# Optimization experiments

Hardware: AMD Instinct MI355X
Metric: run time of the kernel (lower is better)

## Reference

```python
import jax, jax.numpy as jnp
import numpy as np

N_VARS = 512      # code length n (input_output_layer_size)
DV = 4            # variable-node degree
E = N_VARS * DV   # neurons = number of Tanner-graph edges = 2048
B = 8192          # batch of codewords
CLIP_TANH = 10.0
KL_SCALE = 5.0


def _build_masks():
    # edge e belongs to variable node var_idx[e]
    var_idx = np.repeat(np.arange(N_VARS), DV)          # [E]
    same_var = var_idx[:, None] == var_idx[None, :]     # [E,E]
    # v2c (odd->even) mask: edges sharing a variable node, excluding self-edge
    odd2even_mask = (same_var & ~np.eye(E, dtype=bool)).astype(np.float32)
    # skip-connection mask: LLR of variable v feeds every edge incident to v
    skip_mask = (np.arange(N_VARS)[:, None] == var_idx[None, :]).astype(np.float32)  # [n,E]
    return jnp.asarray(odd2even_mask), jnp.asarray(skip_mask)


def setup_inputs() -> dict:
    key = jax.random.key(0)
    k = jax.random.split(key, 6)
    w_odd2even_mask, w_skipconn2even_mask = _build_masks()
    return {
        "x": jax.random.normal(k[0], (B, E), dtype=jnp.float32),
        "llr": jax.random.normal(k[1], (B, N_VARS), dtype=jnp.float32),
        "odd_weights": jax.random.normal(k[2], (E, E), dtype=jnp.float32),
        "llr_weights": jax.random.normal(k[3], (N_VARS, E), dtype=jnp.float32),
        "dropout_logit": jax.random.uniform(k[4], (E,), dtype=jnp.float32),  # torch.rand init
        "u": jax.random.uniform(k[5], (E, E), dtype=jnp.float32),            # ARM uniform noise
        "w_odd2even_mask": w_odd2even_mask,
        "w_skipconn2even_mask": w_skipconn2even_mask,
    }


def reference(x, llr, odd_weights, llr_weights, dropout_logit, u,
              w_odd2even_mask, w_skipconn2even_mask):
    p = jax.nn.sigmoid(dropout_logit)                       # [E], broadcasts over rows of u
    total_mask = w_odd2even_mask * odd_weights              # [E,E]
    # ARM dropout: z ~ (u < sigmoid(logit)), z_tilde ~ (u > sigmoid(-logit))
    z = (u < p).astype(x.dtype)
    z_tilde = (u > jax.nn.sigmoid(-dropout_logit)).astype(x.dtype)
    msgs = x @ (total_mask * z)                             # [B,E]
    msgs_tilde = x @ (total_mask * z_tilde)                 # [B,E]
    llr_term = llr @ (w_skipconn2even_mask * llr_weights)   # [B,E]
    output = jnp.tanh(0.5 * jnp.clip(msgs + llr_term, -CLIP_TANH, CLIP_TANH))
    init_arm_tilde = jnp.tanh(0.5 * jnp.clip(msgs_tilde + llr_term, -CLIP_TANH, CLIP_TANH))
    # KL / entropy regularizer
    scaling1 = (KL_SCALE ** 2 / 2.0) * p                    # [E]
    first_layer_kl = scaling1 * jnp.sum(odd_weights ** 2, axis=1)  # ||W||_2 per row, squared
    H1 = -p * jnp.log(p) - (1.0 - p) * jnp.log(1.0 - p)
    kl_term = jnp.mean(first_layer_kl - H1)
    return output, init_arm_tilde, kl_term
```

## Files before the change

### kernel.cpp

```cpp
#include <hip/hip_runtime.h>
#include <math.h>

#define N_VARS 512
#define DV 4
#define EDGES 2048
#define BATCH 8192
#define CLIP_TANH 10.0f
#define ROWS 8

__global__ __launch_bounds__(256) void precompute_params(
    const float* __restrict__ odd_weights,
    const float* __restrict__ llr_weights,
    const float* __restrict__ dropout_logit,
    const float* __restrict__ u,
    const float* __restrict__ mask_oe,
    const float* __restrict__ mask_skip,
    float4* __restrict__ WZ,
    float4* __restrict__ WZT,
    float*  __restrict__ LW)
{
    int e = blockIdx.x * 256 + threadIdx.x;
    if (e >= EDGES) return;
    int v = e >> 2;
    int base = v << 2;

    float logit = dropout_logit[e];
    float p = 1.0f / (1.0f + expf(-logit));
    float q = 1.0f / (1.0f + expf(logit));

    float wz[4], wzt[4];
#pragma unroll
    for (int j = 0; j < 4; ++j) {
        size_t off = (size_t)(base + j) * EDGES + e;
        float w = odd_weights[off] * mask_oe[off];
        float uu = u[off];
        wz[j]  = (uu < p) ? w : 0.0f;
        wzt[j] = (uu > q) ? w : 0.0f;
    }
    WZ[e]  = make_float4(wz[0], wz[1], wz[2], wz[3]);
    WZT[e] = make_float4(wzt[0], wzt[1], wzt[2], wzt[3]);

    size_t soff = (size_t)v * EDGES + e;
    LW[e] = llr_weights[soff] * mask_skip[soff];
}

__global__ __launch_bounds__(256) void kl_rows(
    const float* __restrict__ odd_weights,
    const float* __restrict__ dropout_logit,
    float* __restrict__ rowv)
{
    int e = blockIdx.x;
    int t = threadIdx.x;
    const float4* row = (const float4*)(odd_weights + (size_t)e * EDGES);
    float s = 0.0f;
#pragma unroll
    for (int i = t; i < EDGES / 4; i += 256) {
        float4 w = row[i];
        s = fmaf(w.x, w.x, s);
        s = fmaf(w.y, w.y, s);
        s = fmaf(w.z, w.z, s);
        s = fmaf(w.w, w.w, s);
    }
#pragma unroll
    for (int off = 32; off > 0; off >>= 1)
        s += __shfl_down(s, off, 64);
    __shared__ float red[4];
    if ((t & 63) == 0) red[t >> 6] = s;
    __syncthreads();
    if (t == 0) {
        float ss = red[0] + red[1] + red[2] + red[3];
        float logit = dropout_logit[e];
        float p = 1.0f / (1.0f + expf(-logit));
        float H1 = -p * logf(p) - (1.0f - p) * logf(1.0f - p);
        rowv[e] = 12.5f * p * ss - H1;
    }
}

__global__ __launch_bounds__(256) void kl_final(
    const float* __restrict__ rowv, float* __restrict__ out)
{
    int t = threadIdx.x;
    float s = 0.0f;
#pragma unroll
    for (int i = t; i < EDGES; i += 256) s += rowv[i];
#pragma unroll
    for (int off = 32; off > 0; off >>= 1)
        s += __shfl_down(s, off, 64);
    __shared__ float red[4];
    if ((t & 63) == 0) red[t >> 6] = s;
    __syncthreads();
    if (t == 0) out[0] = (red[0] + red[1] + red[2] + red[3]) / (float)EDGES;
}

__device__ __forceinline__ float tanh_half(float m) {
    float t = __expf(m);
    return (t - 1.0f) / (t + 1.0f);
}

__global__ __launch_bounds__(256) void main_kernel(
    const float* __restrict__ x,
    const float* __restrict__ llr,
    const float4* __restrict__ WZ,
    const float4* __restrict__ WZT,
    const float*  __restrict__ LW,
    float* __restrict__ out0,
    float* __restrict__ out1)
{
    int idx = blockIdx.x * 256 + threadIdx.x;
    int v = idx & (N_VARS - 1);
    int b0 = (idx >> 9) * ROWS;

    float4 wz[4], wzt[4];
    float lw[4];
#pragma unroll
    for (int c = 0; c < 4; ++c) {
        int e = (v << 2) + c;
        wz[c]  = WZ[e];
        wzt[c] = WZT[e];
        lw[c]  = LW[e];
    }

    float4 x4[ROWS];
    float  l[ROWS];
#pragma unroll
    for (int r = 0; r < ROWS; ++r) {
        x4[r] = ((const float4*)(x + (size_t)(b0 + r) * EDGES))[v];
        l[r]  = llr[(size_t)(b0 + r) * N_VARS + v];
    }

#pragma unroll
    for (int r = 0; r < ROWS; ++r) {
        float o0[4], o1[4];
#pragma unroll
        for (int c = 0; c < 4; ++c) {
            float lt = l[r] * lw[c];
            float m  = fmaf(x4[r].x, wz[c].x,  fmaf(x4[r].y, wz[c].y,
                       fmaf(x4[r].z, wz[c].z,  fmaf(x4[r].w, wz[c].w,  lt))));
            float mt = fmaf(x4[r].x, wzt[c].x, fmaf(x4[r].y, wzt[c].y,
                       fmaf(x4[r].z, wzt[c].z, fmaf(x4[r].w, wzt[c].w, lt))));
            m  = fminf(fmaxf(m,  -CLIP_TANH), CLIP_TANH);
            mt = fminf(fmaxf(mt, -CLIP_TANH), CLIP_TANH);
            o0[c] = tanh_half(m);
            o1[c] = tanh_half(mt);
        }
        ((float4*)(out0 + (size_t)(b0 + r) * EDGES))[v] =
            make_float4(o0[0], o0[1], o0[2], o0[3]);
        ((float4*)(out1 + (size_t)(b0 + r) * EDGES))[v] =
            make_float4(o1[0], o1[1], o1[2], o1[3]);
    }
}

extern "C" void kernel_launch(void* const* d_in, const int* in_sizes, int n_in,
                              void* d_out, int out_size, void* d_ws, size_t ws_size,
                              hipStream_t stream) {
    const float* x             = (const float*)d_in[0];
    const float* llr           = (const float*)d_in[1];
    const float* odd_weights   = (const float*)d_in[2];
    const float* llr_weights   = (const float*)d_in[3];
    const float* dropout_logit = (const float*)d_in[4];
    const float* u             = (const float*)d_in[5];
    const float* mask_oe       = (const float*)d_in[6];
    const float* mask_skip     = (const float*)d_in[7];

    float* out0 = (float*)d_out;
    float* out1 = out0 + (size_t)BATCH * EDGES;
    float* kl   = out0 + (size_t)2 * BATCH * EDGES;

    char* ws = (char*)d_ws;
    float4* WZ  = (float4*)(ws);
    float4* WZT = (float4*)(ws + 32768);
    float*  LW  = (float*) (ws + 65536);
    float*  ROWV= (float*) (ws + 73728);

    precompute_params<<<EDGES / 256, 256, 0, stream>>>(
        odd_weights, llr_weights, dropout_logit, u, mask_oe, mask_skip, WZ, WZT, LW);
    kl_rows<<<EDGES, 256, 0, stream>>>(odd_weights, dropout_logit, ROWV);
    kl_final<<<1, 256, 0, stream>>>(ROWV, kl);

    int threads = (BATCH / ROWS) * N_VARS;
    main_kernel<<<threads / 256, 256, 0, stream>>>(
        x, llr, WZ, WZT, LW, out0, out1);
}
```

Measured before the change: 53.50 us.

## Merge prep kernels, fold KL final reduction into main kernel, use nontemporal memory ops

Fuses the parameter precompute and per-row KL kernels into one launch, using block index ranges to pick the role. The final KL mean reduction moves into block 0 of the main kernel, so there are two launches instead of four. Loads of x and odd_weights and the output stores become nontemporal to reduce cache pollution on streamed data. Risks include the extra work on block 0 of the main kernel and whatever effect the nontemporal hints have on the memory path.

```diff
diff --git a/kernel.cpp b/kernel.cpp
--- a/kernel.cpp
+++ b/kernel.cpp
@@ -8,88 +8,72 @@
 #define CLIP_TANH 10.0f
 #define ROWS 8
 
-__global__ __launch_bounds__(256) void precompute_params(
+typedef float f32x4 __attribute__((ext_vector_type(4)));
+
+__global__ __launch_bounds__(256) void prep_kernel(
     const float* __restrict__ odd_weights,
     const float* __restrict__ llr_weights,
     const float* __restrict__ dropout_logit,
     const float* __restrict__ u,
     const float* __restrict__ mask_oe,
     const float* __restrict__ mask_skip,
-    float4* __restrict__ WZ,
-    float4* __restrict__ WZT,
-    float*  __restrict__ LW)
-{
-    int e = blockIdx.x * 256 + threadIdx.x;
-    if (e >= EDGES) return;
-    int v = e >> 2;
-    int base = v << 2;
-
-    float logit = dropout_logit[e];
-    float p = 1.0f / (1.0f + expf(-logit));
-    float q = 1.0f / (1.0f + expf(logit));
-
-    float wz[4], wzt[4];
-#pragma unroll
-    for (int j = 0; j < 4; ++j) {
-        size_t off = (size_t)(base + j) * EDGES + e;
-        float w = odd_weights[off] * mask_oe[off];
-        float uu = u[off];
-        wz[j]  = (uu < p) ? w : 0.0f;
-        wzt[j] = (uu > q) ? w : 0.0f;
-    }
-    WZ[e]  = make_float4(wz[0], wz[1], wz[2], wz[3]);
-    WZT[e] = make_float4(wzt[0], wzt[1], wzt[2], wzt[3]);
-
-    size_t soff = (size_t)v * EDGES + e;
-    LW[e] = llr_weights[soff] * mask_skip[soff];
-}
-
-__global__ __launch_bounds__(256) void kl_rows(
-    const float* __restrict__ odd_weights,
-    const float* __restrict__ dropout_logit,
+    f32x4* __restrict__ WZ,
+    f32x4* __restrict__ WZT,
+    float* __restrict__ LW,
     float* __restrict__ rowv)
 {
-    int e = blockIdx.x;
+    int blk = blockIdx.x;
     int t = threadIdx.x;
-    const float4* row = (const float4*)(odd_weights + (size_t)e * EDGES);
-    float s = 0.0f;
+
+    if (blk < EDGES) {
+        int e = blk;
+        const f32x4* row = (const f32x4*)(odd_weights + (size_t)e * EDGES);
+        float s = 0.0f;
 #pragma unroll
-    for (int i = t; i < EDGES / 4; i += 256) {
-        float4 w = row[i];
-        s = fmaf(w.x, w.x, s);
-        s = fmaf(w.y, w.y, s);
-        s = fmaf(w.z, w.z, s);
-        s = fmaf(w.w, w.w, s);
-    }
+        for (int i = t; i < EDGES / 4; i += 256) {
+            f32x4 w = __builtin_nontemporal_load(&row[i]);
+            s = fmaf(w.x, w.x, s);
+            s = fmaf(w.y, w.y, s);
+            s = fmaf(w.z, w.z, s);
+            s = fmaf(w.w, w.w, s);
+        }
 #pragma unroll
-    for (int off = 32; off > 0; off >>= 1)
-        s += __shfl_down(s, off, 64);
-    __shared__ float red[4];
-    if ((t & 63) == 0) red[t >> 6] = s;
-    __syncthreads();
-    if (t == 0) {
-        float ss = red[0] + red[1] + red[2] + red[3];
+        for (int off = 32; off > 0; off >>= 1)
+            s += __shfl_down(s, off, 64);
+        __shared__ float red[4];
+        if ((t & 63) == 0) red[t >> 6] = s;
+        __syncthreads();
+        if (t == 0) {
+            float ss = red[0] + red[1] + red[2] + red[3];
+            float logit = dropout_logit[e];
+            float p = 1.0f / (1.0f + expf(-logit));
+            float H1 = -p * logf(p) - (1.0f - p) * logf(1.0f - p);
+            rowv[e] = 12.5f * p * ss - H1;
+        }
+    } else {
+        int e = (blk - EDGES) * 256 + t;
+        int v = e >> 2;
+        int base = v << 2;
+
         float logit = dropout_logit[e];
         float p = 1.0f / (1.0f + expf(-logit));
-        float H1 = -p * logf(p) - (1.0f - p) * logf(1.0f - p);
-        rowv[e] = 12.5f * p * ss - H1;
+        float q = 1.0f / (1.0f + expf(logit));
+
+        f32x4 wz, wzt;
+#pragma unroll
+        for (int j = 0; j < 4; ++j) {
+            size_t off = (size_t)(base + j) * EDGES + e;
+            float w = odd_weights[off] * mask_oe[off];
+            float uu = u[off];
+            wz[j]  = (uu < p) ? w : 0.0f;
+            wzt[j] = (uu > q) ? w : 0.0f;
+        }
+        WZ[e]  = wz;
+        WZT[e] = wzt;
+
+        size_t soff = (size_t)v * EDGES + e;
+        LW[e] = llr_weights[soff] * mask_skip[soff];
     }
-}
-
-__global__ __launch_bounds__(256) void kl_final(
-    const float* __restrict__ rowv, float* __restrict__ out)
-{
-    int t = threadIdx.x;
-    float s = 0.0f;
-#pragma unroll
-    for (int i = t; i < EDGES; i += 256) s += rowv[i];
-#pragma unroll
-    for (int off = 32; off > 0; off >>= 1)
-        s += __shfl_down(s, off, 64);
-    __shared__ float red[4];
-    if ((t & 63) == 0) red[t >> 6] = s;
-    __syncthreads();
-    if (t == 0) out[0] = (red[0] + red[1] + red[2] + red[3]) / (float)EDGES;
 }
 
 __device__ __forceinline__ float tanh_half(float m) {
@@ -100,17 +84,19 @@
 __global__ __launch_bounds__(256) void main_kernel(
     const float* __restrict__ x,
     const float* __restrict__ llr,
-    const float4* __restrict__ WZ,
-    const float4* __restrict__ WZT,
-    const float*  __restrict__ LW,
+    const f32x4* __restrict__ WZ,
+    const f32x4* __restrict__ WZT,
+    const float* __restrict__ LW,
+    const float* __restrict__ rowv,
     float* __restrict__ out0,
-    float* __restrict__ out1)
+    float* __restrict__ out1,
+    float* __restrict__ kl)
 {
     int idx = blockIdx.x * 256 + threadIdx.x;
     int v = idx & (N_VARS - 1);
     int b0 = (idx >> 9) * ROWS;
 
-    float4 wz[4], wzt[4];
+    f32x4 wz[4], wzt[4];
     float lw[4];
 #pragma unroll
     for (int c = 0; c < 4; ++c) {
@@ -120,17 +106,18 @@
         lw[c]  = LW[e];
     }
 
-    float4 x4[ROWS];
-    float  l[ROWS];
+    f32x4 x4[ROWS];
+    float l[ROWS];
 #pragma unroll
     for (int r = 0; r < ROWS; ++r) {
-        x4[r] = ((const float4*)(x + (size_t)(b0 + r) * EDGES))[v];
+        x4[r] = __builtin_nontemporal_load(
+                    &((const f32x4*)(x + (size_t)(b0 + r) * EDGES))[v]);
         l[r]  = llr[(size_t)(b0 + r) * N_VARS + v];
     }
 
 #pragma unroll
     for (int r = 0; r < ROWS; ++r) {
-        float o0[4], o1[4];
+        f32x4 o0, o1;
 #pragma unroll
         for (int c = 0; c < 4; ++c) {
             float lt = l[r] * lw[c];
@@ -143,10 +130,24 @@
             o0[c] = tanh_half(m);
             o1[c] = tanh_half(mt);
         }
-        ((float4*)(out0 + (size_t)(b0 + r) * EDGES))[v] =
-            make_float4(o0[0], o0[1], o0[2], o0[3]);
-        ((float4*)(out1 + (size_t)(b0 + r) * EDGES))[v] =
-            make_float4(o1[0], o1[1], o1[2], o1[3]);
+        __builtin_nontemporal_store(o0,
+            &((f32x4*)(out0 + (size_t)(b0 + r) * EDGES))[v]);
+        __builtin_nontemporal_store(o1,
+            &((f32x4*)(out1 + (size_t)(b0 + r) * EDGES))[v]);
+    }
+
+    if (blockIdx.x == 0) {
+        int t = threadIdx.x;
+        float s = 0.0f;
+#pragma unroll
+        for (int i = t; i < EDGES; i += 256) s += rowv[i];
+#pragma unroll
+        for (int off = 32; off > 0; off >>= 1)
+            s += __shfl_down(s, off, 64);
+        __shared__ float red[4];
+        if ((t & 63) == 0) red[t >> 6] = s;
+        __syncthreads();
+        if (t == 0) kl[0] = (red[0] + red[1] + red[2] + red[3]) / (float)EDGES;
     }
 }
 
@@ -167,17 +168,16 @@
     float* kl   = out0 + (size_t)2 * BATCH * EDGES;
 
     char* ws = (char*)d_ws;
-    float4* WZ  = (float4*)(ws);
-    float4* WZT = (float4*)(ws + 32768);
-    float*  LW  = (float*) (ws + 65536);
-    float*  ROWV= (float*) (ws + 73728);
+    f32x4* WZ  = (f32x4*)(ws);
+    f32x4* WZT = (f32x4*)(ws + 32768);
+    float* LW  = (float*)(ws + 65536);
+    float* ROWV= (float*)(ws + 73728);
 
-    precompute_params<<<EDGES / 256, 256, 0, stream>>>(
-        odd_weights, llr_weights, dropout_logit, u, mask_oe, mask_skip, WZ, WZT, LW);
-    kl_rows<<<EDGES, 256, 0, stream>>>(odd_weights, dropout_logit, ROWV);
-    kl_final<<<1, 256, 0, stream>>>(ROWV, kl);
+    prep_kernel<<<EDGES + EDGES / 256, 256, 0, stream>>>(
+        odd_weights, llr_weights, dropout_logit, u, mask_oe, mask_skip,
+        WZ, WZT, LW, ROWV);
 
     int threads = (BATCH / ROWS) * N_VARS;
     main_kernel<<<threads / 256, 256, 0, stream>>>(
-        x, llr, WZ, WZT, LW, out0, out1);
+        x, llr, WZ, WZT, LW, ROWV, out0, out1, kl);
 }
```

Measured after the change: 57.00 us. 6.5% more time.
